# Kernel tuning notes

Measured on AMD Instinct MI355X. Metric: run time of the kernel, lower is better.

Reference implementation:

```python
import jax, jax.numpy as jnp
import numpy as np

B, N, FD = 8, 32768, 32
NUM_GROUP, GROUP_SIZE = 1024, 32
RAD_FIVE_DEG = 0.087266  # radians_of_five_degrees threshold


def setup_inputs() -> dict:
    key = jax.random.key(0)
    k1, k2, k3 = jax.random.split(key, 3)
    coord = jax.random.normal(k1, (B * N, 3), dtype=jnp.float32)
    feat = jax.random.normal(k2, (B * N, FD), dtype=jnp.float32)
    labels = jax.random.randint(k3, (B * N,), 0, 20)
    offset = jnp.cumsum(jnp.full((B,), N, dtype=jnp.int32))  # [N, 2N, ..., BN]
    return {"coord": coord, "feat": feat, "labels": labels, "offset": offset}


def _fps(coords, num_samples):
    """Farthest point sampling on one cloud. coords: [N,3] -> [num_samples] indices."""
    d = jnp.sum((coords - coords[0]) ** 2, axis=-1)  # dist to first selected point

    def step(dist, _):
        idx = jnp.argmax(dist)
        nd = jnp.sum((coords - coords[idx]) ** 2, axis=-1)
        return jnp.minimum(dist, nd), idx

    _, idxs = jax.lax.scan(step, d, None, length=num_samples - 1)
    return jnp.concatenate([jnp.zeros((1,), dtype=idxs.dtype), idxs])


def reference(coord, feat, labels, offset):
    b = offset.shape[0]
    n = coord.shape[0] // b
    c = coord.reshape(b, n, 3)        # [B,N,3]
    f = feat.reshape(b, n, FD)        # [B,N,FD]
    lab = labels.reshape(b, n)

    # --- FPS: num_group samples per cloud ---
    s_idx = jax.vmap(_fps, in_axes=(0, None))(c, NUM_GROUP)  # [B,G]

    s_xyz = jnp.take_along_axis(c, s_idx[..., None], axis=1)          # [B,G,3]
    s_feat = jnp.take_along_axis(f, s_idx[..., None], axis=1)         # [B,G,FD]
    s_labels = jnp.take_along_axis(lab, s_idx, axis=1)                # [B,G]

    # --- kNN within each cloud: [B,G,N] distance matrix, top-k smallest ---
    d2 = jnp.sum((s_xyz[:, :, None, :] - c[:, None, :, :]) ** 2, axis=-1)  # [B,G,N]
    _, n_idx = jax.lax.top_k(-d2, GROUP_SIZE)                              # [B,G,K] ascending distance

    # gather neighbor features: [B,G,K,FD]
    s_n_feat = jax.vmap(lambda fb, ib: fb[ib])(f, n_idx)

    # --- point curvature: 2*atan2(||a*|b| - |a|*b||, ||a*|b| + |a|*b||) ---
    a = s_feat[:, :, None, :]                                   # [B,G,1,FD]
    an = jnp.linalg.norm(a, axis=-1, keepdims=True)             # [B,G,1,1]
    bn = jnp.linalg.norm(s_n_feat, axis=-1, keepdims=True)      # [B,G,K,1]
    num = jnp.linalg.norm(a * bn - an * s_n_feat, axis=-1)      # [B,G,K]
    den = jnp.linalg.norm(a * bn + an * s_n_feat, axis=-1)      # [B,G,K]
    angles = 2.0 * jnp.arctan2(num, den)                        # [B,G,K]
    # drop self neighbor (first, distance 0), mean over remaining
    p_curv = jnp.mean(angles[:, :, 1:], axis=-1, keepdims=True)  # [B,G,1]

    shape_weight = (p_curv > RAD_FIVE_DEG).astype(jnp.int32).squeeze(-1)  # [B,G]
    feat_out = jnp.concatenate([s_feat, p_curv], axis=-1)                 # [B,G,FD+1]

    # flat index back to parent (global flat indexing, per original flat layout)
    s_idx_flat = s_idx + jnp.arange(b, dtype=s_idx.dtype)[:, None] * n

    return (s_xyz.reshape(-1, 3),
            feat_out.reshape(-1, FD + 1),
            shape_weight.reshape(-1),
            s_labels.reshape(-1),
            s_idx_flat.reshape(-1))
```

## Files before the change

kernel.cpp:

```cpp
#include <hip/hip_runtime.h>
#include <math.h>

#define BATCH   8
#define NPTS    32768
#define FDIM    32
#define NGROUP  1024
#define GSIZE   32
#define KLANE   8

#define NBLK    8
#define FTPB    512
#define CHUNK   (NPTS / NBLK)
#define NFPSBLK (BATCH * NBLK)
#define KNNQPB  8
#define NKNNBLK ((BATCH * NGROUP) / KNNQPB)

__device__ __forceinline__ float dist2f(float ax, float ay, float az,
                                        float bx, float by, float bz) {
  float dx = __fsub_rn(ax, bx);
  float dy = __fsub_rn(ay, by);
  float dz = __fsub_rn(az, bz);
  return __fadd_rn(__fadd_rn(__fmul_rn(dx, dx), __fmul_rn(dy, dy)),
                   __fmul_rn(dz, dz));
}

#define X8(M) M(0) M(1) M(2) M(3) M(4) M(5) M(6) M(7)

__global__ __launch_bounds__(FTPB) void fused_kernel(
    const float* __restrict__ coord, const float* __restrict__ feat,
    const int* __restrict__ labels,
    unsigned long long* __restrict__ slots,
    int* __restrict__ s_idx_ws,
    float* __restrict__ out) {
  __shared__ float redv[8];
  __shared__ int   redp[8];
  __shared__ unsigned long long bcast;

  const int bx   = blockIdx.x;
  const int tid  = threadIdx.x;
  const int lane = tid & 63;
  const int wid  = tid >> 6;

  if (bx < NFPSBLK) {
    const int gb   = bx;
    const int b    = gb & 7;
    const int bk   = gb >> 3;
    const float* __restrict__ c = coord + (size_t)b * NPTS * 3;
    const float3* __restrict__ c3 = (const float3*)c;
    const int pbase = bk * CHUNK + tid;

#define DECL8(i) float x##i, y##i, z##i, d##i;
    X8(DECL8)
#undef DECL8

    float qx = c[0], qy = c[1], qz = c[2];
    float bestv = -1.0f; int bestp = 0;
#define LOAD8(i) { int p = pbase + (i) * FTPB; float3 v = c3[p];            \
    x##i = v.x; y##i = v.y; z##i = v.z;                                      \
    float t2 = dist2f(v.x, v.y, v.z, qx, qy, qz); d##i = t2;                 \
    if (t2 > bestv) { bestv = t2; bestp = p; } }
    X8(LOAD8)
#undef LOAD8

    if (bk == 0 && tid == 0)
      __hip_atomic_store(&s_idx_ws[b * NGROUP + 0], 1, __ATOMIC_RELAXED,
                         __HIP_MEMORY_SCOPE_AGENT);

    for (int t = 1; t < NGROUP; ++t) {
      float v = bestv; int p = bestp;
      #pragma unroll
      for (int m = 1; m < 64; m <<= 1) {
        float ov = __shfl_xor(v, m, 64);
        int   op = __shfl_xor(p, m, 64);
        if (ov > v || (ov == v && op < p)) { v = ov; p = op; }
      }
      if (lane == 0) { redv[wid] = v; redp[wid] = p; }
      __syncthreads();

      if (wid == 0) {
        float gv = redv[lane & 7]; int gp = redp[lane & 7];
        #pragma unroll
        for (int m = 1; m < 8; m <<= 1) {
          float ov = __shfl_xor(gv, m, 64);
          int   op = __shfl_xor(gp, m, 64);
          if (ov > gv || (ov == gv && op < gp)) { gv = ov; gp = op; }
        }
        unsigned long long* base = slots + (size_t)(t & 1) * (BATCH * NBLK);
        if (lane == 0) {
          unsigned long long pk = ((unsigned long long)t << 47)
                                | ((unsigned long long)__float_as_uint(gv) << 15)
                                | (unsigned long long)(0x7FFF - gp);
          __hip_atomic_store(base + (b << 3) + bk, pk, __ATOMIC_RELEASE,
                             __HIP_MEMORY_SCOPE_AGENT);
        }
        unsigned long long pk2 = 0;
        if (lane < 8) {
          const unsigned long long* sl = base + (b << 3) + lane;
          do {
            pk2 = __hip_atomic_load(sl, __ATOMIC_ACQUIRE,
                                    __HIP_MEMORY_SCOPE_AGENT);
          } while ((int)(pk2 >> 47) != t);
        }
        #pragma unroll
        for (int m = 1; m < 8; m <<= 1) {
          unsigned long long o = __shfl_xor(pk2, m, 64);
          if (o > pk2) pk2 = o;
        }
        if (lane == 0) bcast = pk2;
      }
      __syncthreads();

      const unsigned long long wpk = bcast;
      const int gp = 0x7FFF - (int)(wpk & 0x7FFF);
      if (bk == 0 && tid == 0)
        __hip_atomic_store(&s_idx_ws[b * NGROUP + t], gp + 1,
                           __ATOMIC_RELAXED, __HIP_MEMORY_SCOPE_AGENT);
      if (t == NGROUP - 1) break;

      float3 q = c3[gp];
      qx = q.x; qy = q.y; qz = q.z;
      bestv = -1.0f; bestp = 0;
#define UPD8(i) { float t2 = dist2f(x##i, y##i, z##i, qx, qy, qz);           \
    float nd = fminf(d##i, t2); d##i = nd;                                   \
    if (nd > bestv) { bestv = nd; bestp = pbase + (i) * FTPB; } }
      X8(UPD8)
#undef UPD8
    }
    return;
  }

  const int qid = (bx - NFPSBLK) * KNNQPB + wid;
  const int b   = qid >> 10;
  const float* __restrict__ c = coord + (size_t)b * NPTS * 3;

  int enc;
  for (;;) {
    enc = __hip_atomic_load(&s_idx_ws[qid], __ATOMIC_RELAXED,
                            __HIP_MEMORY_SCOPE_AGENT);
    if (enc != 0) break;
    __builtin_amdgcn_s_sleep(16);
  }
  const int sp = __builtin_amdgcn_readfirstlane(enc - 1);
  const int gq = b * NPTS + sp;
  const float qx = coord[(size_t)gq * 3 + 0];
  const float qy = coord[(size_t)gq * 3 + 1];
  const float qz = coord[(size_t)gq * 3 + 2];

  float lv[KLANE]; int li[KLANE];
  #pragma unroll
  for (int j = 0; j < KLANE; ++j) { lv[j] = 1e30f; li[j] = 0x7fffffff; }

#define INSERT(D2, P) \
  if ((D2) < lv[KLANE - 1]) { \
    _Pragma("unroll") \
    for (int j = KLANE - 1; j >= 1; --j) { \
      bool up = (D2) < lv[j - 1]; \
      float nv = up ? lv[j - 1] : (((D2) < lv[j]) ? (D2) : lv[j]); \
      int   ni = up ? li[j - 1] : (((D2) < lv[j]) ? (P)  : li[j]); \
      lv[j] = nv; li[j] = ni; \
    } \
    if ((D2) < lv[0]) { lv[0] = (D2); li[0] = (P); } \
  }

  for (int s = 0; s < NPTS / 256; ++s) {
    int p = (s << 8) | (lane << 2);
    const float4* c4 = (const float4*)(c + (size_t)p * 3);
    float4 f0 = c4[0], f1 = c4[1], f2 = c4[2];
    float dA = dist2f(f0.x, f0.y, f0.z, qx, qy, qz);
    float dB = dist2f(f0.w, f1.x, f1.y, qx, qy, qz);
    float dC = dist2f(f1.z, f1.w, f2.x, qx, qy, qz);
    float dD = dist2f(f2.y, f2.z, f2.w, qx, qy, qz);
    INSERT(dA, p);
    INSERT(dB, p + 1);
    INSERT(dC, p + 2);
    INSERT(dD, p + 3);
  }
#undef INSERT

  int nbp = 0;
  for (int r = 0; r < GSIZE; ++r) {
    float mv = lv[0]; int mp = li[0];
    #pragma unroll
    for (int m = 1; m < 64; m <<= 1) {
      float ov = __shfl_xor(mv, m, 64);
      int   op = __shfl_xor(mp, m, 64);
      if (ov < mv || (ov == mv && op < mp)) { mv = ov; mp = op; }
    }
    if (lane == r) nbp = mp;
    if (lv[0] == mv && li[0] == mp) {
      #pragma unroll
      for (int j = 0; j < KLANE - 1; ++j) { lv[j] = lv[j + 1]; li[j] = li[j + 1]; }
      lv[KLANE - 1] = 1e30f; li[KLANE - 1] = 0x7fffffff;
    }
  }

  const float* aRow = feat + (size_t)gq * FDIM;
  float my_a = (lane < FDIM) ? aRow[lane] : 0.0f;

  float ang = 0.0f;
  if (lane >= 1 && lane < GSIZE) {
    const float4* a4 = (const float4*)aRow;
    const float4* b4 = (const float4*)(feat + ((size_t)b * NPTS + nbp) * FDIM);
    float4 av[FDIM / 4], bv[FDIM / 4];
    float aa = 0.0f, bb = 0.0f;
    #pragma unroll
    for (int k = 0; k < FDIM / 4; ++k) {
      av[k] = a4[k]; bv[k] = b4[k];
      aa += av[k].x * av[k].x + av[k].y * av[k].y + av[k].z * av[k].z + av[k].w * av[k].w;
      bb += bv[k].x * bv[k].x + bv[k].y * bv[k].y + bv[k].z * bv[k].z + bv[k].w * bv[k].w;
    }
    float an = sqrtf(aa), bn = sqrtf(bb);
    float num2 = 0.0f, den2 = 0.0f;
    #pragma unroll
    for (int k = 0; k < FDIM / 4; ++k) {
      float n0 = av[k].x * bn - an * bv[k].x, dd0 = av[k].x * bn + an * bv[k].x;
      float n1 = av[k].y * bn - an * bv[k].y, dd1 = av[k].y * bn + an * bv[k].y;
      float n2 = av[k].z * bn - an * bv[k].z, dd2 = av[k].z * bn + an * bv[k].z;
      float n3 = av[k].w * bn - an * bv[k].w, dd3 = av[k].w * bn + an * bv[k].w;
      num2 += n0 * n0 + n1 * n1 + n2 * n2 + n3 * n3;
      den2 += dd0 * dd0 + dd1 * dd1 + dd2 * dd2 + dd3 * dd3;
    }
    ang = 2.0f * atan2f(sqrtf(num2), sqrtf(den2));
  }

  float tot = ang;
  #pragma unroll
  for (int m = 1; m < 64; m <<= 1) tot += __shfl_xor(tot, m, 64);
  float p_curv = tot / 31.0f;

  float* out_xyz  = out;
  float* out_feat = out + (size_t)BATCH * NGROUP * 3;
  float* out_sw   = out_feat + (size_t)BATCH * NGROUP * (FDIM + 1);
  float* out_lab  = out_sw  + (size_t)BATCH * NGROUP;
  float* out_sif  = out_lab + (size_t)BATCH * NGROUP;

  if (lane < FDIM)  out_feat[(size_t)qid * (FDIM + 1) + lane] = my_a;
  if (lane == FDIM) out_feat[(size_t)qid * (FDIM + 1) + FDIM] = p_curv;
  if (lane == 0) {
    out_xyz[(size_t)qid * 3 + 0] = qx;
    out_xyz[(size_t)qid * 3 + 1] = qy;
    out_xyz[(size_t)qid * 3 + 2] = qz;
    out_sw[qid]  = (p_curv > 0.087266f) ? 1.0f : 0.0f;
    out_lab[qid] = (float)labels[gq];
    out_sif[qid] = (float)gq;
  }
}

extern "C" void kernel_launch(void* const* d_in, const int* in_sizes, int n_in,
                              void* d_out, int out_size, void* d_ws, size_t ws_size,
                              hipStream_t stream) {
  const float* coord  = (const float*)d_in[0];
  const float* feat   = (const float*)d_in[1];
  const int*   labels = (const int*)d_in[2];

  unsigned long long* slots = (unsigned long long*)d_ws;
  int* s_idx_ws = (int*)((char*)d_ws +
                         2 * BATCH * NBLK * sizeof(unsigned long long));
  const size_t zbytes = 2 * BATCH * NBLK * sizeof(unsigned long long)
                      + (size_t)BATCH * NGROUP * sizeof(int);

  hipMemsetAsync(d_ws, 0, zbytes, stream);
  fused_kernel<<<NFPSBLK + NKNNBLK, FTPB, 0, stream>>>(
      coord, feat, labels, slots, s_idx_ws, (float*)d_out);
}
```

Before: 2.928 ms.

## Replace per-block slot exchange with atomic max plus counter barrier in FPS

Each FPS block now publishes its local argmax with an atomic fetch_max into a shared per-batch cell and bumps a per-batch arrival counter, instead of writing its own slot and having wave 0 poll all eight slots and reduce them. Every thread then spins on the counter and reads the reduced cell directly, which removes one __syncthreads and the LDS broadcast from each of the 1023 iterations. kNN waiters also sleep longer in proportion to their group index to cut polling traffic while FPS runs. The costs are that all 512 threads per block now poll global memory, which adds contention, and the cells are reused by parity, so their correctness relies on the counter ordering.

```diff
diff --git a/kernel.cpp b/kernel.cpp
--- a/kernel.cpp
+++ b/kernel.cpp
@@ -29,12 +29,12 @@
 __global__ __launch_bounds__(FTPB) void fused_kernel(
     const float* __restrict__ coord, const float* __restrict__ feat,
     const int* __restrict__ labels,
-    unsigned long long* __restrict__ slots,
+    unsigned long long* __restrict__ maxcell,
+    unsigned int* __restrict__ cnt,
     int* __restrict__ s_idx_ws,
     float* __restrict__ out) {
   __shared__ float redv[8];
   __shared__ int   redp[8];
-  __shared__ unsigned long long bcast;
 
   const int bx   = blockIdx.x;
   const int tid  = threadIdx.x;
@@ -42,9 +42,8 @@
   const int wid  = tid >> 6;
 
   if (bx < NFPSBLK) {
-    const int gb   = bx;
-    const int b    = gb & 7;
-    const int bk   = gb >> 3;
+    const int b    = bx & 7;
+    const int bk   = bx >> 3;
     const float* __restrict__ c = coord + (size_t)b * NPTS * 3;
     const float3* __restrict__ c3 = (const float3*)c;
     const int pbase = bk * CHUNK + tid;
@@ -65,6 +64,8 @@
     if (bk == 0 && tid == 0)
       __hip_atomic_store(&s_idx_ws[b * NGROUP + 0], 1, __ATOMIC_RELAXED,
                          __HIP_MEMORY_SCOPE_AGENT);
+
+    unsigned int* mycnt = cnt + b * 32;
 
     for (int t = 1; t < NGROUP; ++t) {
       float v = bestv; int p = bestp;
@@ -77,6 +78,7 @@
       if (lane == 0) { redv[wid] = v; redp[wid] = p; }
       __syncthreads();
 
+      unsigned long long* cell = maxcell + ((size_t)(t & 1) * BATCH + b) * 16;
       if (wid == 0) {
         float gv = redv[lane & 7]; int gp = redp[lane & 7];
         #pragma unroll
@@ -85,34 +87,29 @@
           int   op = __shfl_xor(gp, m, 64);
           if (ov > gv || (ov == gv && op < gp)) { gv = ov; gp = op; }
         }
-        unsigned long long* base = slots + (size_t)(t & 1) * (BATCH * NBLK);
         if (lane == 0) {
           unsigned long long pk = ((unsigned long long)t << 47)
                                 | ((unsigned long long)__float_as_uint(gv) << 15)
                                 | (unsigned long long)(0x7FFF - gp);
-          __hip_atomic_store(base + (b << 3) + bk, pk, __ATOMIC_RELEASE,
-                             __HIP_MEMORY_SCOPE_AGENT);
+          __hip_atomic_fetch_max(cell, pk, __ATOMIC_RELAXED,
+                                 __HIP_MEMORY_SCOPE_AGENT);
+          __hip_atomic_fetch_add(mycnt, 1u, __ATOMIC_RELEASE,
+                                 __HIP_MEMORY_SCOPE_AGENT);
         }
-        unsigned long long pk2 = 0;
-        if (lane < 8) {
-          const unsigned long long* sl = base + (b << 3) + lane;
-          do {
-            pk2 = __hip_atomic_load(sl, __ATOMIC_ACQUIRE,
-                                    __HIP_MEMORY_SCOPE_AGENT);
-          } while ((int)(pk2 >> 47) != t);
-        }
-        #pragma unroll
-        for (int m = 1; m < 8; m <<= 1) {
-          unsigned long long o = __shfl_xor(pk2, m, 64);
-          if (o > pk2) pk2 = o;
-        }
-        if (lane == 0) bcast = pk2;
       }
-      __syncthreads();
-
-      const unsigned long long wpk = bcast;
+
+      const unsigned int tgt = 8u * (unsigned int)t;
+      unsigned int cv;
+      do {
+        cv = __hip_atomic_load(mycnt, __ATOMIC_RELAXED,
+                               __HIP_MEMORY_SCOPE_AGENT);
+      } while (cv < tgt);
+      (void)__hip_atomic_load(mycnt, __ATOMIC_ACQUIRE,
+                              __HIP_MEMORY_SCOPE_AGENT);
+      unsigned long long wpk = __hip_atomic_load(cell, __ATOMIC_RELAXED,
+                                                 __HIP_MEMORY_SCOPE_AGENT);
       const int gp = 0x7FFF - (int)(wpk & 0x7FFF);
-      if (bk == 0 && tid == 0)
+      if (bk == 0 && wid == 0 && lane == 0)
         __hip_atomic_store(&s_idx_ws[b * NGROUP + t], gp + 1,
                            __ATOMIC_RELAXED, __HIP_MEMORY_SCOPE_AGENT);
       if (t == NGROUP - 1) break;
@@ -133,12 +130,18 @@
   const int b   = qid >> 10;
   const float* __restrict__ c = coord + (size_t)b * NPTS * 3;
 
-  int enc;
-  for (;;) {
+  const int tq = qid & (NGROUP - 1);
+  int enc = __hip_atomic_load(&s_idx_ws[qid], __ATOMIC_RELAXED,
+                              __HIP_MEMORY_SCOPE_AGENT);
+  for (int i = (tq * 3) >> 2; i > 0 && enc == 0; --i) {
+    __builtin_amdgcn_s_sleep(127);
     enc = __hip_atomic_load(&s_idx_ws[qid], __ATOMIC_RELAXED,
                             __HIP_MEMORY_SCOPE_AGENT);
-    if (enc != 0) break;
+  }
+  while (enc == 0) {
     __builtin_amdgcn_s_sleep(16);
+    enc = __hip_atomic_load(&s_idx_ws[qid], __ATOMIC_RELAXED,
+                            __HIP_MEMORY_SCOPE_AGENT);
   }
   const int sp = __builtin_amdgcn_readfirstlane(enc - 1);
   const int gq = b * NPTS + sp;
@@ -253,13 +256,13 @@
   const float* feat   = (const float*)d_in[1];
   const int*   labels = (const int*)d_in[2];
 
-  unsigned long long* slots = (unsigned long long*)d_ws;
-  int* s_idx_ws = (int*)((char*)d_ws +
-                         2 * BATCH * NBLK * sizeof(unsigned long long));
-  const size_t zbytes = 2 * BATCH * NBLK * sizeof(unsigned long long)
+  unsigned long long* maxcell = (unsigned long long*)d_ws;
+  unsigned int* cnt = (unsigned int*)((char*)d_ws + 2 * BATCH * 16 * 8);
+  int* s_idx_ws = (int*)((char*)d_ws + 2 * BATCH * 16 * 8 + BATCH * 32 * 4);
+  const size_t zbytes = 2 * BATCH * 16 * 8 + BATCH * 32 * 4
                       + (size_t)BATCH * NGROUP * sizeof(int);
 
   hipMemsetAsync(d_ws, 0, zbytes, stream);
   fused_kernel<<<NFPSBLK + NKNNBLK, FTPB, 0, stream>>>(
-      coord, feat, labels, slots, s_idx_ws, (float*)d_out);
+      coord, feat, labels, maxcell, cnt, s_idx_ws, (float*)d_out);
 }
```

After: 7.250 ms. +147.6%, slower.
